# Kernel tuning notes

Hardware: AMD Instinct MI355X
Metric: run time of the kernel (lower is better)

Reference implementation:

```python
import jax, jax.numpy as jnp
import numpy as np

N_NODES = 50000
N_EDGES = 800000
F_IN = 128
HEADS = 4
C_OUT = 32
NEG_SLOPE = 0.2
BN_EPS = 1e-5


def _add_self_loops(edge_index, edge_attr, n):
    # PyG fill_value='mean': self-loop attr = mean of incoming edge attrs per node (0 if none)
    src, dst = edge_index[0], edge_index[1]
    deg = jax.ops.segment_sum(jnp.ones_like(edge_attr[:, 0]), dst, num_segments=n)
    loop_attr = jax.ops.segment_sum(edge_attr, dst, num_segments=n) / jnp.maximum(deg, 1.0)[:, None]
    loop = jnp.arange(n)
    src2 = jnp.concatenate([src, loop])
    dst2 = jnp.concatenate([dst, loop])
    attr2 = jnp.concatenate([edge_attr, loop_attr], axis=0)
    return src2, dst2, attr2


def _segment_softmax(logits, seg, n):
    m = jax.ops.segment_max(logits, seg, num_segments=n)
    m = jnp.where(jnp.isfinite(m), m, 0.0)
    ex = jnp.exp(logits - m[seg])
    s = jax.ops.segment_sum(ex, seg, num_segments=n)
    return ex / s[seg]


def _gatv2(x, src, dst, eattr, Wl, bl, Wr, br, We, att, bias, n):
    # x: [n, F]; returns [n, HEADS*C_OUT]
    xl = (x @ Wl + bl).reshape(n, HEADS, C_OUT)
    xr = (x @ Wr + br).reshape(n, HEADS, C_OUT)
    ea = (eattr @ We).reshape(-1, HEADS, C_OUT)
    xlj = xl[src]                                   # [E, H, C] gather
    msg = jax.nn.leaky_relu(xlj + xr[dst] + ea, NEG_SLOPE)
    logits = jnp.einsum('ehc,hc->eh', msg, att)     # [E, H]
    alpha = _segment_softmax(logits, dst, n)
    out = jax.ops.segment_sum(xlj * alpha[..., None], dst, num_segments=n)
    return out.reshape(n, HEADS * C_OUT) + bias


def _batchnorm(x, gamma, beta):
    mu = x.mean(axis=0)
    var = x.var(axis=0)
    return gamma * (x - mu) * jax.lax.rsqrt(var + BN_EPS) + beta


def setup_inputs() -> dict:
    key = jax.random.key(0)
    ks = jax.random.split(key, 20)
    HC = HEADS * C_OUT
    s = 0.05
    inp = {
        'emb': jax.random.normal(ks[0], (N_NODES, F_IN), dtype=jnp.float32),
        'edge_index': jax.random.randint(ks[1], (2, N_EDGES), 0, N_NODES, dtype=jnp.int64),
        'edge_weight': jax.random.uniform(ks[2], (N_EDGES, 1), dtype=jnp.float32),
        'Wl1': jax.random.normal(ks[3], (F_IN, HC)) * s,
        'bl1': jnp.zeros((HC,), jnp.float32),
        'Wr1': jax.random.normal(ks[4], (F_IN, HC)) * s,
        'br1': jnp.zeros((HC,), jnp.float32),
        'We1': jax.random.normal(ks[5], (1, HC)) * s,
        'att1': jax.random.normal(ks[6], (HEADS, C_OUT)) * s,
        'bias1': jnp.zeros((HC,), jnp.float32),
        'gamma1': jnp.ones((HC,), jnp.float32),
        'beta1': jnp.zeros((HC,), jnp.float32),
        'Wl2': jax.random.normal(ks[7], (HC, HC)) * s,
        'bl2': jnp.zeros((HC,), jnp.float32),
        'Wr2': jax.random.normal(ks[8], (HC, HC)) * s,
        'br2': jnp.zeros((HC,), jnp.float32),
        'We2': jax.random.normal(ks[9], (1, HC)) * s,
        'att2': jax.random.normal(ks[10], (HEADS, C_OUT)) * s,
        'bias2': jnp.zeros((HC,), jnp.float32),
    }
    return inp


def reference(emb, edge_index, edge_weight, Wl1, bl1, Wr1, br1, We1, att1, bias1,
              gamma1, beta1, Wl2, bl2, Wr2, br2, We2, att2, bias2):
    n = emb.shape[0]
    src, dst, eattr = _add_self_loops(edge_index, edge_weight, n)
    h1 = _gatv2(emb, src, dst, eattr, Wl1, bl1, Wr1, br1, We1, att1, bias1, n)
    h1 = jax.nn.elu(_batchnorm(h1, gamma1, beta1))
    h2 = _gatv2(h1, src, dst, eattr, Wl2, bl2, Wr2, br2, We2, att2, bias2, n)
    # fusion: mean over [input_emb, h1, h2] along stacked axis
    return (emb + h1 + h2) / 3.0
```

## Files before the change

kernel.cpp:

```cpp
#include <hip/hip_runtime.h>
#include <hip/hip_bf16.h>
#include <math.h>

#define N_NODES 50000
#define N_EDGES 800000
#define HC 128
#define SLOT 64
#define CSTRIDE 16

#define BM 128
#define NBX ((N_NODES + BM - 1) / BM)

typedef short bh8 __attribute__((ext_vector_type(8)));
typedef float f4 __attribute__((ext_vector_type(4)));
typedef float f2 __attribute__((ext_vector_type(2)));

__device__ __forceinline__ unsigned int pk2(float a, float b) {
  return (unsigned int)__bfloat16_as_ushort(__float2bfloat16(a)) |
         ((unsigned int)__bfloat16_as_ushort(__float2bfloat16(b)) << 16);
}
__device__ __forceinline__ float blo(unsigned int u) { return __uint_as_float(u << 16); }
__device__ __forceinline__ float bhi(unsigned int u) { return __uint_as_float(u & 0xffff0000u); }

__global__ __launch_bounds__(256) void k_wprep(
    const float* __restrict__ Wl1, const float* __restrict__ Wr1,
    const float* __restrict__ Wl2, const float* __restrict__ Wr2,
    unsigned short* __restrict__ WtAll, int* __restrict__ cursor,
    float* __restrict__ chsum, float* __restrict__ chsq) {
  int gid = blockIdx.x * 256 + threadIdx.x;
  int m = gid >> 14;
  int idx = gid & 16383;
  const float* src = (m == 0) ? Wl1 : (m == 1) ? Wr1 : (m == 2) ? Wl2 : Wr2;
  int k = idx >> 7, n = idx & 127;
  WtAll[((size_t)m * HC + n) * HC + k] =
      __bfloat16_as_ushort(__float2bfloat16(src[k * HC + n]));
  for (int i = gid; i < N_NODES * CSTRIDE; i += 65536) cursor[i] = 0;
  if (gid < HC) { chsum[gid] = 0.f; chsq[gid] = 0.f; }
}

__global__ __launch_bounds__(256) void k_g1prep(
    const float* __restrict__ X, const unsigned short* __restrict__ Wt,
    const float* __restrict__ b0, const float* __restrict__ b1,
    unsigned short* __restrict__ Y0b, float* __restrict__ Y1,
    const int* __restrict__ ei, const float* __restrict__ ew,
    int* __restrict__ cursor, unsigned int* __restrict__ slots) {
  __shared__ __align__(16) unsigned short Xls[128 * 128];
  __shared__ __align__(16) unsigned short Wls[128 * 128];
  int bid = blockIdx.x;
  int tid = threadIdx.x;

  int et = bid * 256 + tid;
  bool has_e = (et < N_EDGES / 8);
  int e0 = et * 8;
  int ss[8], dd[8];
  float ww[8];
  int pos[8];
  if (has_e) {
    *(int4*)&ss[0] = *(const int4*)(ei + e0);
    *(int4*)&ss[4] = *(const int4*)(ei + e0 + 4);
    *(int4*)&dd[0] = *(const int4*)(ei + N_EDGES + e0);
    *(int4*)&dd[4] = *(const int4*)(ei + N_EDGES + e0 + 4);
    *(float4*)&ww[0] = *(const float4*)(ew + e0);
    *(float4*)&ww[4] = *(const float4*)(ew + e0 + 4);
#pragma unroll
    for (int i = 0; i < 8; ++i) pos[i] = atomicAdd(cursor + dd[i] * CSTRIDE, 1);
  }

  int row0 = bid * BM;
  {
    int r = tid >> 1;
    int ks = (tid & 1) * 64;
    int gr = row0 + r;
    const float* xp = X + (size_t)gr * HC + ks;
    int sw = r & 15;
#pragma unroll
    for (int i = 0; i < 4; ++i) {
      float f[16];
      if (gr < N_NODES) {
        *(float4*)&f[0] = *(const float4*)(xp + i * 16);
        *(float4*)&f[4] = *(const float4*)(xp + i * 16 + 4);
        *(float4*)&f[8] = *(const float4*)(xp + i * 16 + 8);
        *(float4*)&f[12] = *(const float4*)(xp + i * 16 + 12);
      } else {
#pragma unroll
        for (int j = 0; j < 16; ++j) f[j] = 0.f;
      }
      int kg = (ks >> 3) + i * 2;
      *(uint4*)&Xls[r * 128 + ((kg ^ sw) * 8)] =
          make_uint4(pk2(f[0], f[1]), pk2(f[2], f[3]), pk2(f[4], f[5]), pk2(f[6], f[7]));
      *(uint4*)&Xls[r * 128 + (((kg + 1) ^ sw) * 8)] =
          make_uint4(pk2(f[8], f[9]), pk2(f[10], f[11]), pk2(f[12], f[13]), pk2(f[14], f[15]));
    }
  }

  if (has_e) {
#pragma unroll
    for (int i = 0; i < 8; ++i) {
      unsigned int wq = min((unsigned int)(ww[i] * 65536.f + 0.5f), 65535u);
      if (pos[i] < SLOT) {
        slots[(size_t)dd[i] * SLOT + pos[i]] = ((unsigned int)ss[i] << 16) | wq;
      }
    }
  }

  int lane = tid & 63;
  int wv = tid >> 6;
  int lrow = lane & 15;
  int lq = lane >> 4;
  int rbase = wv * 32;
#pragma unroll
  for (int half = 0; half < 2; ++half) {
    if (half) __syncthreads();
    {
      int n = tid >> 1;
      int ks2 = (tid & 1) * 64;
      const unsigned short* wp = Wt + half * (HC * HC) + n * HC + ks2;
      int swn = n & 15;
#pragma unroll
      for (int g = 0; g < 8; ++g) {
        uint4 v = *(const uint4*)(wp + g * 8);
        int kg = (ks2 >> 3) + g;
        *(uint4*)&Wls[n * 128 + ((kg ^ swn) * 8)] = v;
      }
    }
    __syncthreads();
    f4 acc[2][8];
#pragma unroll
    for (int mt = 0; mt < 2; ++mt)
#pragma unroll
      for (int nt = 0; nt < 8; ++nt) acc[mt][nt] = (f4){0.f, 0.f, 0.f, 0.f};
#pragma unroll
    for (int kk = 0; kk < 4; ++kk) {
      int kg = kk * 4 + lq;
      bh8 a0 = *(const bh8*)&Xls[(rbase + lrow) * 128 + ((kg ^ lrow) * 8)];
      bh8 a1 = *(const bh8*)&Xls[(rbase + 16 + lrow) * 128 + ((kg ^ lrow) * 8)];
#pragma unroll
      for (int nt = 0; nt < 8; ++nt) {
        bh8 b = *(const bh8*)&Wls[(nt * 16 + lrow) * 128 + ((kg ^ lrow) * 8)];
        acc[0][nt] = __builtin_amdgcn_mfma_f32_16x16x32_bf16(a0, b, acc[0][nt], 0, 0, 0);
        acc[1][nt] = __builtin_amdgcn_mfma_f32_16x16x32_bf16(a1, b, acc[1][nt], 0, 0, 0);
      }
    }
    const float* bb = half ? b1 : b0;
    float bv[8];
#pragma unroll
    for (int nt = 0; nt < 8; ++nt) bv[nt] = bb[nt * 16 + lrow];
#pragma unroll
    for (int mt = 0; mt < 2; ++mt) {
#pragma unroll
      for (int rr = 0; rr < 4; ++rr) {
        int gr = row0 + rbase + mt * 16 + lq * 4 + rr;
        if (gr < N_NODES) {
          if (half == 0) {
#pragma unroll
            for (int nt = 0; nt < 8; ++nt)
              Y0b[(size_t)gr * HC + nt * 16 + lrow] =
                  __bfloat16_as_ushort(__float2bfloat16(acc[mt][nt][rr] + bv[nt]));
          } else {
#pragma unroll
            for (int nt = 0; nt < 8; ++nt)
              Y1[(size_t)gr * HC + nt * 16 + lrow] = acc[mt][nt][rr] + bv[nt];
          }
        }
      }
    }
  }
}

__global__ __launch_bounds__(256) void k_gemm2(
    const unsigned short* __restrict__ Xb, const unsigned short* __restrict__ Wt,
    const float* __restrict__ b0, const float* __restrict__ b1,
    unsigned char* __restrict__ Y0f8, float* __restrict__ Y1,
    const float* __restrict__ chsum, const float* __restrict__ chsq,
    const float* __restrict__ gamma, const float* __restrict__ beta) {
  __shared__ __align__(16) unsigned short Xls[128 * 128];
  __shared__ __align__(16) unsigned short Wls[128 * 128];
  __shared__ float ssc[HC], ssh[HC];
  int tid = threadIdx.x;
  if (tid < HC) {
    float mu = chsum[tid] * (1.f / N_NODES);
    float var = chsq[tid] * (1.f / N_NODES) - mu * mu;
    float sc = gamma[tid] * rsqrtf(var + 1e-5f);
    ssc[tid] = sc;
    ssh[tid] = beta[tid] - mu * sc;
  }
  __syncthreads();
  int row0 = blockIdx.x * BM;
  {
    int r = tid >> 1;
    int ks = (tid & 1) * 64;
    int gr = row0 + r;
    const unsigned short* xp = Xb + (size_t)gr * HC + ks;
    int sw = r & 15;
#pragma unroll
    for (int i = 0; i < 4; ++i) {
      float f[16];
      if (gr < N_NODES) {
        uint4 ua = *(const uint4*)(xp + i * 16);
        uint4 ub = *(const uint4*)(xp + i * 16 + 8);
        f[0] = blo(ua.x); f[1] = bhi(ua.x); f[2] = blo(ua.y); f[3] = bhi(ua.y);
        f[4] = blo(ua.z); f[5] = bhi(ua.z); f[6] = blo(ua.w); f[7] = bhi(ua.w);
        f[8] = blo(ub.x); f[9] = bhi(ub.x); f[10] = blo(ub.y); f[11] = bhi(ub.y);
        f[12] = blo(ub.z); f[13] = bhi(ub.z); f[14] = blo(ub.w); f[15] = bhi(ub.w);
      } else {
#pragma unroll
        for (int j = 0; j < 16; ++j) f[j] = 0.f;
      }
#pragma unroll
      for (int j = 0; j < 16; ++j) {
        float y = fmaf(f[j], ssc[ks + i * 16 + j], ssh[ks + i * 16 + j]);
        f[j] = (y > 0.f) ? y : (__expf(y) - 1.f);
      }
      int kg = (ks >> 3) + i * 2;
      *(uint4*)&Xls[r * 128 + ((kg ^ sw) * 8)] =
          make_uint4(pk2(f[0], f[1]), pk2(f[2], f[3]), pk2(f[4], f[5]), pk2(f[6], f[7]));
      *(uint4*)&Xls[r * 128 + (((kg + 1) ^ sw) * 8)] =
          make_uint4(pk2(f[8], f[9]), pk2(f[10], f[11]), pk2(f[12], f[13]), pk2(f[14], f[15]));
    }
  }
  int lane = tid & 63;
  int wv = tid >> 6;
  int lrow = lane & 15;
  int lq = lane >> 4;
  int rbase = wv * 32;
#pragma unroll
  for (int half = 0; half < 2; ++half) {
    if (half) __syncthreads();
    {
      int n = tid >> 1;
      int ks = (tid & 1) * 64;
      const unsigned short* wp = Wt + half * (HC * HC) + n * HC + ks;
      int swn = n & 15;
#pragma unroll
      for (int g = 0; g < 8; ++g) {
        uint4 v = *(const uint4*)(wp + g * 8);
        int kg = (ks >> 3) + g;
        *(uint4*)&Wls[n * 128 + ((kg ^ swn) * 8)] = v;
      }
    }
    __syncthreads();
    f4 acc[2][8];
#pragma unroll
    for (int mt = 0; mt < 2; ++mt)
#pragma unroll
      for (int nt = 0; nt < 8; ++nt) acc[mt][nt] = (f4){0.f, 0.f, 0.f, 0.f};
#pragma unroll
    for (int kk = 0; kk < 4; ++kk) {
      int kg = kk * 4 + lq;
      bh8 a0 = *(const bh8*)&Xls[(rbase + lrow) * 128 + ((kg ^ lrow) * 8)];
      bh8 a1 = *(const bh8*)&Xls[(rbase + 16 + lrow) * 128 + ((kg ^ lrow) * 8)];
#pragma unroll
      for (int nt = 0; nt < 8; ++nt) {
        bh8 b = *(const bh8*)&Wls[(nt * 16 + lrow) * 128 + ((kg ^ lrow) * 8)];
        acc[0][nt] = __builtin_amdgcn_mfma_f32_16x16x32_bf16(a0, b, acc[0][nt], 0, 0, 0);
        acc[1][nt] = __builtin_amdgcn_mfma_f32_16x16x32_bf16(a1, b, acc[1][nt], 0, 0, 0);
      }
    }
    const float* bb = half ? b1 : b0;
    float bv[8];
#pragma unroll
    for (int nt = 0; nt < 8; ++nt) bv[nt] = bb[nt * 16 + lrow];
#pragma unroll
    for (int mt = 0; mt < 2; ++mt) {
#pragma unroll
      for (int rr = 0; rr < 4; ++rr) {
        int gr = row0 + rbase + mt * 16 + lq * 4 + rr;
        if (gr < N_NODES) {
          if (half == 0) {
#pragma unroll
            for (int nt = 0; nt < 8; ++nt) {
              float v = acc[mt][nt][rr] + bv[nt];
              int p = __builtin_amdgcn_cvt_pk_fp8_f32(v, v, 0, false);
              Y0f8[(size_t)gr * HC + nt * 16 + lrow] = (unsigned char)(p & 0xff);
            }
          } else {
#pragma unroll
            for (int nt = 0; nt < 8; ++nt)
              Y1[(size_t)gr * HC + nt * 16 + lrow] = acc[mt][nt][rr] + bv[nt];
          }
        }
      }
    }
  }
}

template <int FINAL, int F8>
__global__ __launch_bounds__(256) void k_gat(
    const void* __restrict__ xlv, const float* __restrict__ xr,
    const int* __restrict__ cursor, const unsigned int* __restrict__ slots,
    const float* __restrict__ We, const float* __restrict__ att,
    const float* __restrict__ bias, void* __restrict__ out,
    const float* __restrict__ emb, const unsigned short* __restrict__ h1p,
    const float* __restrict__ chsum, const float* __restrict__ chsq,
    const float* __restrict__ gamma, const float* __restrict__ beta) {
  int g = threadIdx.x >> 5;
  int lane = threadIdx.x & 31;
  int n = blockIdx.x * 8 + g;
  int fi = n * 32 + lane;
  const uint2* xl2 = (const uint2*)xlv;
  const unsigned int* xf = (const unsigned int*)xlv;
  float4 xr4 = ((const float4*)xr)[fi];
  float4 we4 = ((const float4*)We)[lane];
  float4 at4 = ((const float4*)att)[lane];
  int deg = min(cursor[n * CSTRIDE], SLOT);
  int base = n * SLOT;
  int deg32 = min(deg, 32);

  unsigned int ev = (lane < deg32) ? slots[base + lane] : 0u;
  float evw = (float)(ev & 0xffffu) * (1.f / 65536.f);
  float wsum = evw;
#pragma unroll
  for (int m = 16; m >= 1; m >>= 1) wsum += __shfl_xor(wsum, m);

  float l = 0.f;
  float4 o = make_float4(0.f, 0.f, 0.f, 0.f);

  auto decode = [&](uint2 gc) -> float4 {
    float4 xlj;
    if (F8) {
      f2 ab = __builtin_amdgcn_cvt_pk_f32_fp8((int)gc.x, false);
      f2 cd = __builtin_amdgcn_cvt_pk_f32_fp8((int)gc.x, true);
      xlj.x = ab[0]; xlj.y = ab[1]; xlj.z = cd[0]; xlj.w = cd[1];
    } else {
      xlj.x = blo(gc.x); xlj.y = bhi(gc.x);
      xlj.z = blo(gc.y); xlj.w = bhi(gc.y);
    }
    return xlj;
  };
  auto edge_body = [&](float w, uint2 gc, bool valid) {
    float4 xlj = decode(gc);
    float4 v;
    v.x = fmaf(w, we4.x, xlj.x + xr4.x);
    v.y = fmaf(w, we4.y, xlj.y + xr4.y);
    v.z = fmaf(w, we4.z, xlj.z + xr4.z);
    v.w = fmaf(w, we4.w, xlj.w + xr4.w);
    v.x = fmaxf(v.x, 0.2f * v.x);
    v.y = fmaxf(v.y, 0.2f * v.y);
    v.z = fmaxf(v.z, 0.2f * v.z);
    v.w = fmaxf(v.w, 0.2f * v.w);
    float p = v.x * at4.x + v.y * at4.y + v.z * at4.z + v.w * at4.w;
    p += __shfl_xor(p, 1);
    p += __shfl_xor(p, 2);
    p += __shfl_xor(p, 4);
    float e = valid ? __expf(p) : 0.f;
    l += e;
    o.x = fmaf(e, xlj.x, o.x);
    o.y = fmaf(e, xlj.y, o.y);
    o.z = fmaf(e, xlj.z, o.z);
    o.w = fmaf(e, xlj.w, o.w);
  };
  auto fetch = [&](int j, uint2& qq, float& ww) {
    int jc = min(j, deg32 - 1);
    unsigned int evj = __shfl(ev, jc, 32);
    ww = (float)(evj & 0xffffu) * (1.f / 65536.f);
    int s = (int)(evj >> 16);
    if (F8) qq.x = xf[s * 32 + lane];
    else qq = xl2[s * 32 + lane];
  };

  if (deg32 > 0) {
    uint2 q0, q1, q2, q3;
    float w0, w1, w2, w3;
    fetch(0, q0, w0);
    fetch(1, q1, w1);
    fetch(2, q2, w2);
    fetch(3, q3, w3);
    for (int b = 0; b < deg32; b += 4) {
      uint2 c0 = q0, c1 = q1, c2 = q2, c3 = q3;
      float x0 = w0, x1 = w1, x2 = w2, x3 = w3;
      fetch(b + 4, q0, w0);
      fetch(b + 5, q1, w1);
      fetch(b + 6, q2, w2);
      fetch(b + 7, q3, w3);
      edge_body(x0, c0, true);
      edge_body(x1, c1, b + 1 < deg32);
      edge_body(x2, c2, b + 2 < deg32);
      edge_body(x3, c3, b + 3 < deg32);
    }
  }
  if (deg > 32) {
    for (int j = base + 32; j < base + deg; ++j) {
      unsigned int evj = slots[j];
      float w = (float)(evj & 0xffffu) * (1.f / 65536.f);
      wsum += w;
      int s = (int)(evj >> 16);
      uint2 gc;
      if (F8) gc.x = xf[s * 32 + lane];
      else gc = xl2[s * 32 + lane];
      edge_body(w, gc, true);
    }
  }
  {
    float wself = (deg > 0) ? wsum / (float)deg : 0.f;
    uint2 gs;
    if (F8) gs.x = xf[n * 32 + lane];
    else gs = xl2[n * 32 + lane];
    edge_body(wself, gs, true);
  }

  float inv = 1.f / l;
  float4 b4 = ((const float4*)bias)[lane];
  float4 r;
  r.x = fmaf(o.x, inv, b4.x);
  r.y = fmaf(o.y, inv, b4.y);
  r.z = fmaf(o.z, inv, b4.z);
  r.w = fmaf(o.w, inv, b4.w);
  if (FINAL) {
    float4 e4 = ((const float4*)emb)[fi];
    uint2 hh = ((const uint2*)h1p)[fi];
    float4 h4;
    h4.x = blo(hh.x); h4.y = bhi(hh.x); h4.z = blo(hh.y); h4.w = bhi(hh.y);
    float4 cs = ((const float4*)chsum)[lane];
    float4 cq = ((const float4*)chsq)[lane];
    float4 gm = ((const float4*)gamma)[lane];
    float4 bt = ((const float4*)beta)[lane];
    const float invN = 1.f / N_NODES;
    float4 sc4, sh4;
    {
      float mu = cs.x * invN, var = cq.x * invN - mu * mu;
      sc4.x = gm.x * rsqrtf(var + 1e-5f); sh4.x = bt.x - mu * sc4.x;
      mu = cs.y * invN; var = cq.y * invN - mu * mu;
      sc4.y = gm.y * rsqrtf(var + 1e-5f); sh4.y = bt.y - mu * sc4.y;
      mu = cs.z * invN; var = cq.z * invN - mu * mu;
      sc4.z = gm.z * rsqrtf(var + 1e-5f); sh4.z = bt.z - mu * sc4.z;
      mu = cs.w * invN; var = cq.w * invN - mu * mu;
      sc4.w = gm.w * rsqrtf(var + 1e-5f); sh4.w = bt.w - mu * sc4.w;
    }
    float4 h;
    h.x = fmaf(h4.x, sc4.x, sh4.x);
    h.y = fmaf(h4.y, sc4.y, sh4.y);
    h.z = fmaf(h4.z, sc4.z, sh4.z);
    h.w = fmaf(h4.w, sc4.w, sh4.w);
    h.x = (h.x > 0.f) ? h.x : (__expf(h.x) - 1.f);
    h.y = (h.y > 0.f) ? h.y : (__expf(h.y) - 1.f);
    h.z = (h.z > 0.f) ? h.z : (__expf(h.z) - 1.f);
    h.w = (h.w > 0.f) ? h.w : (__expf(h.w) - 1.f);
    const float k3 = 1.f / 3.f;
    r.x = (e4.x + h.x + r.x) * k3;
    r.y = (e4.y + h.y + r.y) * k3;
    r.z = (e4.z + h.z + r.z) * k3;
    r.w = (e4.w + h.w + r.w) * k3;
    ((float4*)out)[fi] = r;
  } else {
    ((uint2*)out)[fi] = make_uint2(pk2(r.x, r.y), pk2(r.z, r.w));
  }
}

#define BN_ROWS 200
__global__ __launch_bounds__(256) void k_bnstats(const unsigned short* __restrict__ h1b,
                                                 float* __restrict__ chsum,
                                                 float* __restrict__ chsq) {
  int c2 = threadIdx.x & 63;
  int g = threadIdx.x >> 6;
  int r0 = blockIdx.x * BN_ROWS;
  float s0 = 0.f, s1 = 0.f, q0 = 0.f, q1 = 0.f;
  const unsigned int* h32 = (const unsigned int*)h1b;
  for (int r = r0 + g; r < r0 + BN_ROWS; r += 4) {
    unsigned int u = h32[(size_t)r * 64 + c2];
    float a = blo(u), b = bhi(u);
    s0 += a; q0 += a * a;
    s1 += b; q1 += b * b;
  }
  __shared__ float sh[256][4];
  sh[threadIdx.x][0] = s0; sh[threadIdx.x][1] = q0;
  sh[threadIdx.x][2] = s1; sh[threadIdx.x][3] = q1;
  __syncthreads();
  if (g == 0) {
    float ts0 = 0.f, tq0 = 0.f, ts1 = 0.f, tq1 = 0.f;
#pragma unroll
    for (int gg = 0; gg < 4; ++gg) {
      ts0 += sh[gg * 64 + c2][0]; tq0 += sh[gg * 64 + c2][1];
      ts1 += sh[gg * 64 + c2][2]; tq1 += sh[gg * 64 + c2][3];
    }
    atomicAdd(chsum + 2 * c2, ts0);
    atomicAdd(chsq + 2 * c2, tq0);
    atomicAdd(chsum + 2 * c2 + 1, ts1);
    atomicAdd(chsq + 2 * c2 + 1, tq1);
  }
}

extern "C" void kernel_launch(void* const* d_in, const int* in_sizes, int n_in,
                              void* d_out, int out_size, void* d_ws, size_t ws_size,
                              hipStream_t stream) {
  const float* emb = (const float*)d_in[0];
  const int* ei = (const int*)d_in[1];
  const float* ew = (const float*)d_in[2];
  const float* Wl1 = (const float*)d_in[3];
  const float* bl1 = (const float*)d_in[4];
  const float* Wr1 = (const float*)d_in[5];
  const float* br1 = (const float*)d_in[6];
  const float* We1 = (const float*)d_in[7];
  const float* att1 = (const float*)d_in[8];
  const float* bias1 = (const float*)d_in[9];
  const float* gamma1 = (const float*)d_in[10];
  const float* beta1 = (const float*)d_in[11];
  const float* Wl2 = (const float*)d_in[12];
  const float* bl2 = (const float*)d_in[13];
  const float* Wr2 = (const float*)d_in[14];
  const float* br2 = (const float*)d_in[15];
  const float* We2 = (const float*)d_in[16];
  const float* att2 = (const float*)d_in[17];
  const float* bias2 = (const float*)d_in[18];
  float* out = (float*)d_out;

  char* wsb = (char*)d_ws;
  size_t off = 0;
  auto alloc = [&](size_t bytes) -> void* {
    void* p = (void*)(wsb + off);
    off += (bytes + 255) & ~(size_t)255;
    return p;
  };
  int* cursor = (int*)alloc((size_t)N_NODES * CSTRIDE * 4);
  float* chsum = (float*)alloc(HC * 4);
  float* chsq = (float*)alloc(HC * 4);
  unsigned short* WtAll = (unsigned short*)alloc((size_t)4 * HC * HC * 2);
  unsigned int* slots = (unsigned int*)alloc((size_t)N_NODES * SLOT * 4);
  unsigned short* xlb = (unsigned short*)alloc((size_t)N_NODES * HC * 2);
  unsigned char* xlf8 = (unsigned char*)alloc((size_t)N_NODES * HC);
  float* xr = (float*)alloc((size_t)N_NODES * HC * 4);
  unsigned short* h1b = (unsigned short*)alloc((size_t)N_NODES * HC * 2);

  k_wprep<<<256, 256, 0, stream>>>(Wl1, Wr1, Wl2, Wr2, WtAll, cursor, chsum, chsq);
  k_g1prep<<<NBX, 256, 0, stream>>>(emb, WtAll, bl1, br1, xlb, xr,
                                    ei, ew, cursor, slots);
  k_gat<0, 0><<<N_NODES / 8, 256, 0, stream>>>(xlb, xr, cursor, slots, We1, att1,
                                               bias1, (void*)h1b, nullptr, nullptr,
                                               nullptr, nullptr, nullptr, nullptr);
  k_bnstats<<<N_NODES / BN_ROWS, 256, 0, stream>>>(h1b, chsum, chsq);
  k_gemm2<<<NBX, 256, 0, stream>>>(h1b, WtAll + 2 * HC * HC, bl2, br2, xlf8, xr,
                                   chsum, chsq, gamma1, beta1);
  k_gat<1, 1><<<N_NODES / 8, 256, 0, stream>>>(xlf8, xr, cursor, slots, We2, att2,
                                               bias2, (void*)out, emb, h1b,
                                               chsum, chsq, gamma1, beta1);
}
```

Measured before the change: 295.2 us.

## Replace global atomic edge bucketing with LDS histogram, scan, and scatter

Edge bucketing by destination no longer uses global atomics on a padded per-node cursor. It now runs three steps: per-chunk LDS histograms with two 16-bit counters packed per word, a per-node scan over 64 chunks that produces chunk base offsets and degrees, and a scatter that uses LDS atomics seeded with those bases. The scatter shares its launch with the first GEMM. This removes contended global atomics and the cursor zeroing, but adds two kernel launches and about 12.8MB of count and base arrays. The scatter needs 100KB of LDS per block, which limits occupancy for the GEMM blocks that share the kernel.

```diff
diff --git a/kernel.cpp b/kernel.cpp
--- a/kernel.cpp
+++ b/kernel.cpp
@@ -6,10 +6,12 @@
 #define N_EDGES 800000
 #define HC 128
 #define SLOT 64
-#define CSTRIDE 16
 
 #define BM 128
 #define NBX ((N_NODES + BM - 1) / BM)
+#define NBKT 64
+#define EPB (N_EDGES / NBKT)
+#define NW (N_NODES / 2)
 
 typedef short bh8 __attribute__((ext_vector_type(8)));
 typedef float f4 __attribute__((ext_vector_type(4)));
@@ -25,7 +27,7 @@
 __global__ __launch_bounds__(256) void k_wprep(
     const float* __restrict__ Wl1, const float* __restrict__ Wr1,
     const float* __restrict__ Wl2, const float* __restrict__ Wr2,
-    unsigned short* __restrict__ WtAll, int* __restrict__ cursor,
+    unsigned short* __restrict__ WtAll,
     float* __restrict__ chsum, float* __restrict__ chsq) {
   int gid = blockIdx.x * 256 + threadIdx.x;
   int m = gid >> 14;
@@ -34,39 +36,81 @@
   int k = idx >> 7, n = idx & 127;
   WtAll[((size_t)m * HC + n) * HC + k] =
       __bfloat16_as_ushort(__float2bfloat16(src[k * HC + n]));
-  for (int i = gid; i < N_NODES * CSTRIDE; i += 65536) cursor[i] = 0;
   if (gid < HC) { chsum[gid] = 0.f; chsq[gid] = 0.f; }
 }
 
-__global__ __launch_bounds__(256) void k_g1prep(
+__global__ __launch_bounds__(1024) void k_hist(const int* __restrict__ ei,
+                                               unsigned int* __restrict__ counts32) {
+  __shared__ unsigned int hist[NW];
+  int tid = threadIdx.x, b = blockIdx.x;
+  for (int w = tid; w < NW; w += 1024) hist[w] = 0u;
+  __syncthreads();
+  const int* dstp = ei + N_EDGES + b * EPB;
+  for (int g = tid; g < EPB / 4; g += 1024) {
+    int4 d4 = *(const int4*)(dstp + g * 4);
+    atomicAdd(&hist[d4.x >> 1], (d4.x & 1) ? 0x10000u : 1u);
+    atomicAdd(&hist[d4.y >> 1], (d4.y & 1) ? 0x10000u : 1u);
+    atomicAdd(&hist[d4.z >> 1], (d4.z & 1) ? 0x10000u : 1u);
+    atomicAdd(&hist[d4.w >> 1], (d4.w & 1) ? 0x10000u : 1u);
+  }
+  __syncthreads();
+  unsigned int* dst = counts32 + (size_t)b * NW;
+  for (int w = tid; w < NW; w += 1024) dst[w] = hist[w];
+}
+
+__global__ __launch_bounds__(256) void k_scan(const unsigned int* __restrict__ counts32,
+                                              unsigned int* __restrict__ bases32,
+                                              int* __restrict__ cursor) {
+  int w = blockIdx.x * 256 + threadIdx.x;
+  if (w >= NW) return;
+  unsigned int a0 = 0, a1 = 0;
+#pragma unroll 4
+  for (int b = 0; b < NBKT; ++b) {
+    unsigned int v = counts32[(size_t)b * NW + w];
+    bases32[(size_t)b * NW + w] = a0 | (a1 << 16);
+    a0 += v & 0xffffu;
+    a1 += v >> 16;
+  }
+  cursor[2 * w] = (int)a0;
+  cursor[2 * w + 1] = (int)a1;
+}
+
+__global__ __launch_bounds__(256) void k_scat_g1(
+    const int* __restrict__ ei, const float* __restrict__ ew,
+    const unsigned int* __restrict__ bases32, unsigned int* __restrict__ slots,
     const float* __restrict__ X, const unsigned short* __restrict__ Wt,
     const float* __restrict__ b0, const float* __restrict__ b1,
-    unsigned short* __restrict__ Y0b, float* __restrict__ Y1,
-    const int* __restrict__ ei, const float* __restrict__ ew,
-    int* __restrict__ cursor, unsigned int* __restrict__ slots) {
-  __shared__ __align__(16) unsigned short Xls[128 * 128];
-  __shared__ __align__(16) unsigned short Wls[128 * 128];
-  int bid = blockIdx.x;
-  int tid = threadIdx.x;
-
-  int et = bid * 256 + tid;
-  bool has_e = (et < N_EDGES / 8);
-  int e0 = et * 8;
-  int ss[8], dd[8];
-  float ww[8];
-  int pos[8];
-  if (has_e) {
-    *(int4*)&ss[0] = *(const int4*)(ei + e0);
-    *(int4*)&ss[4] = *(const int4*)(ei + e0 + 4);
-    *(int4*)&dd[0] = *(const int4*)(ei + N_EDGES + e0);
-    *(int4*)&dd[4] = *(const int4*)(ei + N_EDGES + e0 + 4);
-    *(float4*)&ww[0] = *(const float4*)(ew + e0);
-    *(float4*)&ww[4] = *(const float4*)(ew + e0 + 4);
-#pragma unroll
-    for (int i = 0; i < 8; ++i) pos[i] = atomicAdd(cursor + dd[i] * CSTRIDE, 1);
-  }
-
-  int row0 = bid * BM;
+    unsigned short* __restrict__ Y0b, float* __restrict__ Y1) {
+  __shared__ __align__(16) unsigned int lsbuf[NW];
+  int tid = threadIdx.x, bid = blockIdx.x;
+  if (bid < NBKT) {
+    const unsigned int* bp = bases32 + (size_t)bid * NW;
+    for (int w = tid; w < NW; w += 256) lsbuf[w] = bp[w];
+    __syncthreads();
+    const int* sp = ei + bid * EPB;
+    const int* dp = ei + N_EDGES + bid * EPB;
+    const float* wp = ew + bid * EPB;
+    for (int g = tid; g < EPB / 4; g += 256) {
+      int4 s4 = *(const int4*)(sp + g * 4);
+      int4 d4 = *(const int4*)(dp + g * 4);
+      float4 w4 = *(const float4*)(wp + g * 4);
+      int ss[4] = {s4.x, s4.y, s4.z, s4.w};
+      int dd[4] = {d4.x, d4.y, d4.z, d4.w};
+      float ww[4] = {w4.x, w4.y, w4.z, w4.w};
+#pragma unroll
+      for (int i = 0; i < 4; ++i) {
+        unsigned int old = atomicAdd(&lsbuf[dd[i] >> 1], (dd[i] & 1) ? 0x10000u : 1u);
+        unsigned int pos = (dd[i] & 1) ? (old >> 16) : (old & 0xffffu);
+        unsigned int wq = min((unsigned int)(ww[i] * 65536.f + 0.5f), 65535u);
+        if (pos < SLOT)
+          slots[(size_t)dd[i] * SLOT + pos] = ((unsigned int)ss[i] << 16) | wq;
+      }
+    }
+    return;
+  }
+  unsigned short* Xls = (unsigned short*)lsbuf;
+  unsigned short* Wls = Xls + 128 * 128;
+  int row0 = (bid - NBKT) * BM;
   {
     int r = tid >> 1;
     int ks = (tid & 1) * 64;
@@ -92,17 +136,6 @@
           make_uint4(pk2(f[8], f[9]), pk2(f[10], f[11]), pk2(f[12], f[13]), pk2(f[14], f[15]));
     }
   }
-
-  if (has_e) {
-#pragma unroll
-    for (int i = 0; i < 8; ++i) {
-      unsigned int wq = min((unsigned int)(ww[i] * 65536.f + 0.5f), 65535u);
-      if (pos[i] < SLOT) {
-        slots[(size_t)dd[i] * SLOT + pos[i]] = ((unsigned int)ss[i] << 16) | wq;
-      }
-    }
-  }
-
   int lane = tid & 63;
   int wv = tid >> 6;
   int lrow = lane & 15;
@@ -302,7 +335,7 @@
   float4 xr4 = ((const float4*)xr)[fi];
   float4 we4 = ((const float4*)We)[lane];
   float4 at4 = ((const float4*)att)[lane];
-  int deg = min(cursor[n * CSTRIDE], SLOT);
+  int deg = min(cursor[n], SLOT);
   int base = n * SLOT;
   int deg32 = min(deg, 32);
 
@@ -510,19 +543,23 @@
     off += (bytes + 255) & ~(size_t)255;
     return p;
   };
-  int* cursor = (int*)alloc((size_t)N_NODES * CSTRIDE * 4);
+  int* cursor = (int*)alloc((size_t)N_NODES * 4);
   float* chsum = (float*)alloc(HC * 4);
   float* chsq = (float*)alloc(HC * 4);
   unsigned short* WtAll = (unsigned short*)alloc((size_t)4 * HC * HC * 2);
+  unsigned int* counts32 = (unsigned int*)alloc((size_t)NBKT * NW * 4);
+  unsigned int* bases32 = (unsigned int*)alloc((size_t)NBKT * NW * 4);
   unsigned int* slots = (unsigned int*)alloc((size_t)N_NODES * SLOT * 4);
   unsigned short* xlb = (unsigned short*)alloc((size_t)N_NODES * HC * 2);
   unsigned char* xlf8 = (unsigned char*)alloc((size_t)N_NODES * HC);
   float* xr = (float*)alloc((size_t)N_NODES * HC * 4);
   unsigned short* h1b = (unsigned short*)alloc((size_t)N_NODES * HC * 2);
 
-  k_wprep<<<256, 256, 0, stream>>>(Wl1, Wr1, Wl2, Wr2, WtAll, cursor, chsum, chsq);
-  k_g1prep<<<NBX, 256, 0, stream>>>(emb, WtAll, bl1, br1, xlb, xr,
-                                    ei, ew, cursor, slots);
+  k_wprep<<<256, 256, 0, stream>>>(Wl1, Wr1, Wl2, Wr2, WtAll, chsum, chsq);
+  k_hist<<<NBKT, 1024, 0, stream>>>(ei, counts32);
+  k_scan<<<(NW + 255) / 256, 256, 0, stream>>>(counts32, bases32, cursor);
+  k_scat_g1<<<NBKT + NBX, 256, 0, stream>>>(ei, ew, bases32, slots, emb, WtAll,
+                                            bl1, br1, xlb, xr);
   k_gat<0, 0><<<N_NODES / 8, 256, 0, stream>>>(xlb, xr, cursor, slots, We1, att1,
                                                bias1, (void*)h1b, nullptr, nullptr,
                                                nullptr, nullptr, nullptr, nullptr);
```

Result: faster. 278.5 us (-5.7%).
